# Performance work log

Hardware: AMD Instinct MI355X
Metric: run time of the kernel (lower is better)

The kernel has to match this reference:

```python
import jax, jax.numpy as jnp
import numpy as np

E, K, H, F = 64, 6, 2048, 768        # experts, top_k, hidden, moe_intermediate
G, KG = 8, 4                          # n_group, topk_group
SHARED_F = 768                        # moe_intermediate_size * num_shared_experts
SCALE = 2.5                           # routed_scaling_factor
T = 2 * 1024                          # flattened tokens
CAP = 2 * (T * K // E)


def setup_inputs() -> dict:
    key = jax.random.key(0)
    ks = jax.random.split(key, 9)
    s = 0.02
    return dict(
        hidden_states=jax.random.normal(ks[0], (2, 1024, H), jnp.float32),
        gate_w=jax.random.normal(ks[1], (H, E), jnp.float32) * s,
        bias=jax.random.normal(ks[2], (E,), jnp.float32) * s,          # e_score_correction_bias
        w_gate=jax.random.normal(ks[3], (E, H, F), jnp.float32) * s,
        w_up=jax.random.normal(ks[4], (E, H, F), jnp.float32) * s,
        w_down=jax.random.normal(ks[5], (E, F, H), jnp.float32) * s,
        ws_gate=jax.random.normal(ks[6], (H, SHARED_F), jnp.float32) * s,
        ws_up=jax.random.normal(ks[7], (H, SHARED_F), jnp.float32) * s,
        ws_down=jax.random.normal(ks[8], (SHARED_F, H), jnp.float32) * s,
    )


def _grouped_topk(logits, bias):
    # vLLM grouped_topk with scoring_func='sigmoid' and e_score_correction_bias
    scores = jax.nn.sigmoid(logits.astype(jnp.float32))          # [T, E] original scores
    scores_b = scores + bias[None, :]                            # biased scores for selection
    # group score = sum of top-2 biased scores within each group (bias path)
    gs = scores_b.reshape(-1, G, E // G)
    group_scores = jnp.sum(jax.lax.top_k(gs, 2)[0], axis=-1)     # [T, G]
    gidx = jax.lax.top_k(group_scores, KG)[1]                    # [T, KG]
    rows = jnp.arange(group_scores.shape[0])[:, None]
    group_mask = jnp.zeros_like(group_scores).at[rows, gidx].set(1.0)
    score_mask = jnp.repeat(group_mask, E // G, axis=-1) > 0     # [T, E]
    tmp = jnp.where(score_mask, scores_b, -jnp.inf)
    topk_ids = jax.lax.top_k(tmp, K)[1]                          # [T, K]
    topk_w = jnp.take_along_axis(scores, topk_ids, axis=-1)      # weights from UNBIASED scores
    topk_w = topk_w / jnp.sum(topk_w, axis=-1, keepdims=True)    # renormalize (norm_topk_prob)
    return topk_w * SCALE, topk_ids


def _routed_moe(x, topk_w, topk_ids, w_gate, w_up, w_down):
    Tn = x.shape[0]
    flat_e = topk_ids.reshape(-1)                                # [T*K]
    order = jnp.argsort(flat_e)                                  # stable sort by expert
    se = flat_e[order]                                           # sorted expert ids
    pos = jnp.arange(Tn * K) - jnp.searchsorted(se, se, side='left')  # slot within expert
    tok = order // K                                             # source token per pair
    valid = pos < CAP
    slot = jnp.where(valid, pos, CAP)                            # overflow -> scratch slot
    buf = jnp.zeros((E, CAP + 1, H), x.dtype).at[se, slot].set(x[tok])[:, :CAP]
    h = jax.nn.silu(jnp.einsum('ech,ehf->ecf', buf, w_gate)) * jnp.einsum('ech,ehf->ecf', buf, w_up)
    out = jnp.einsum('ecf,efh->ech', h, w_down)                  # [E, CAP, H]
    gathered = out[se, jnp.minimum(pos, CAP - 1)] * valid.astype(x.dtype)[:, None]
    w = topk_w.reshape(-1)[order].astype(x.dtype)[:, None]
    return jax.ops.segment_sum(gathered * w, tok, num_segments=Tn)


def reference(hidden_states, gate_w, bias, w_gate, w_up, w_down, ws_gate, ws_up, ws_down):
    orig_shape = hidden_states.shape
    x = hidden_states.reshape(-1, H)                             # [T, H]
    router_logits = x @ gate_w                                   # ReplicatedLinear, no bias
    topk_w, topk_ids = _grouped_topk(router_logits, bias)
    y = _routed_moe(x, topk_w, topk_ids, w_gate, w_up, w_down)
    # shared experts: SwiGLU gated MLP
    shared = (jax.nn.silu(x @ ws_gate) * (x @ ws_up)) @ ws_down
    return (y + shared).reshape(orig_shape)
```

## Files before the change

kernel.cpp:

```cpp
#include <hip/hip_runtime.h>
#include <math.h>


#define TOK 2048
#define HD 2048
#define NE 64
#define FD 768
#define TKK 6
#define CAPE 384
#define NG 8
#define KGG 4

typedef float f32x4 __attribute__((ext_vector_type(4)));
typedef short s16x8 __attribute__((ext_vector_type(8)));
typedef short s16x4 __attribute__((ext_vector_type(4)));

__device__ __forceinline__ short f2bf(float f){
  unsigned u = __float_as_uint(f);
  u += 0x7FFFu + ((u >> 16) & 1u);
  return (short)(u >> 16);
}

__global__ void k_convert(const float* __restrict__ x, short* __restrict__ xbf){
  int i = blockIdx.x * 256 + threadIdx.x;
  f32x4 v = ((const f32x4*)x)[i];
  s16x4 o = { f2bf(v[0]), f2bf(v[1]), f2bf(v[2]), f2bf(v[3]) };
  ((s16x4*)xbf)[i] = o;
}

__global__ void k_router(const float* __restrict__ x, const float* __restrict__ gw,
                         float* __restrict__ logits){
  const int t = blockIdx.x * 4 + (threadIdx.x >> 6);
  const int e = threadIdx.x & 63;
  const float* xr = x + (size_t)t * HD;
  float acc = 0.f;
  for (int h = 0; h < HD; h += 4){
    f32x4 xv = *(const f32x4*)(xr + h);
    acc = fmaf(xv[0], gw[(h + 0) * NE + e], acc);
    acc = fmaf(xv[1], gw[(h + 1) * NE + e], acc);
    acc = fmaf(xv[2], gw[(h + 2) * NE + e], acc);
    acc = fmaf(xv[3], gw[(h + 3) * NE + e], acc);
  }
  logits[t * NE + e] = acc;
}

__global__ void k_topk(const float* __restrict__ logits, const float* __restrict__ bias,
                       int* __restrict__ cnt, int* __restrict__ tokl, float* __restrict__ wl){
  const int t = blockIdx.x * 256 + threadIdx.x;
  float sc[NE], sb[NE];
  for (int e = 0; e < NE; ++e){
    float l = logits[t * NE + e];
    float s = 1.f / (1.f + expf(-l));
    sc[e] = s; sb[e] = s + bias[e];
  }
  float gs[NG];
  for (int g = 0; g < NG; ++g){
    float m1 = -1e30f, m2 = -1e30f;
    for (int q = 0; q < 8; ++q){
      float v = sb[g * 8 + q];
      if (v > m1){ m2 = m1; m1 = v; } else if (v > m2){ m2 = v; }
    }
    gs[g] = m1 + m2;
  }
  unsigned gm = 0; unsigned long long allow = 0;
  for (int r = 0; r < KGG; ++r){
    float bb = -1e30f; int bg = 0;
    for (int g = 0; g < NG; ++g)
      if (!((gm >> g) & 1u) && gs[g] > bb){ bb = gs[g]; bg = g; }
    gm |= 1u << bg; allow |= 0xFFull << (bg * 8);
  }
  unsigned long long used = 0; int ids[TKK]; float wv[TKK]; float wsum = 0.f;
  for (int r = 0; r < TKK; ++r){
    float bb = -1e30f; int bi = 0;
    for (int e = 0; e < NE; ++e)
      if (((allow >> e) & 1ull) && !((used >> e) & 1ull) && sb[e] > bb){ bb = sb[e]; bi = e; }
    used |= 1ull << bi; ids[r] = bi;
    float w = sc[bi]; wv[r] = w; wsum += w;
  }
  const float scl = 2.5f / wsum;
  for (int r = 0; r < TKK; ++r){
    int e = ids[r];
    int slot = atomicAdd(cnt + e, 1);
    if (slot < CAPE){ tokl[e * CAPE + slot] = t; wl[e * CAPE + slot] = wv[r] * scl; }
  }
}

template<bool GATHER>
__global__ __launch_bounds__(256, 2) void k_dual(
    const short* __restrict__ xbf,
    const float* __restrict__ Wg, const float* __restrict__ Wu,
    short* __restrict__ hout,
    const int* __restrict__ cnt, const int* __restrict__ tokl)
{
  __shared__ short Asm[256][72];
  __shared__ short Bgs[64][72];
  __shared__ short Bus[64][72];
  const int tid = threadIdx.x;
  const int n0 = blockIdx.x * 64;
  const int m0 = blockIdx.y * 256;
  const int e  = GATHER ? (int)blockIdx.z : 0;
  const int cntc = GATHER ? min(cnt[e], CAPE) : TOK;
  if (m0 >= cntc) return;
  const size_t wb = (size_t)e * HD * FD;
  const float* wg = Wg + wb;
  const float* wu = Wu + wb;

  const int a_r = tid >> 3, a_c = tid & 7;
  const short* arow[8];
#pragma unroll
  for (int p = 0; p < 8; ++p){
    const int gr = m0 + p * 32 + a_r;
    const short* s = nullptr;
    if (gr < cntc){
      const int row = GATHER ? tokl[e * CAPE + gr] : gr;
      s = xbf + (size_t)row * HD;
    }
    arow[p] = s;
  }
  const int b_kg = tid >> 4, b_ng = tid & 15;
  const int lane = tid & 63, wv = tid >> 6;
  const int lm = lane & 15, quad = lane >> 4;

  f32x4 ag[4][4], au[4][4];
#pragma unroll
  for (int i = 0; i < 4; ++i)
#pragma unroll
    for (int j = 0; j < 4; ++j){
      ag[i][j] = {0.f, 0.f, 0.f, 0.f};
      au[i][j] = {0.f, 0.f, 0.f, 0.f};
    }

  for (int k0 = 0; k0 < HD; k0 += 64){
    __syncthreads();
#pragma unroll
    for (int p = 0; p < 8; ++p){
      s16x8 v = {0, 0, 0, 0, 0, 0, 0, 0};
      if (arow[p]) v = *(const s16x8*)(arow[p] + k0 + a_c * 8);
      *(s16x8*)&Asm[p * 32 + a_r][a_c * 8] = v;
    }
    {
      const float* src = wg + (size_t)(k0 + b_kg * 4) * FD + n0 + b_ng * 4;
      f32x4 r0 = *(const f32x4*)(src);
      f32x4 r1 = *(const f32x4*)(src + FD);
      f32x4 r2 = *(const f32x4*)(src + 2 * FD);
      f32x4 r3 = *(const f32x4*)(src + 3 * FD);
#pragma unroll
      for (int c = 0; c < 4; ++c){
        s16x4 v = { f2bf(r0[c]), f2bf(r1[c]), f2bf(r2[c]), f2bf(r3[c]) };
        *(s16x4*)&Bgs[b_ng * 4 + c][b_kg * 4] = v;
      }
      src = wu + (size_t)(k0 + b_kg * 4) * FD + n0 + b_ng * 4;
      r0 = *(const f32x4*)(src);
      r1 = *(const f32x4*)(src + FD);
      r2 = *(const f32x4*)(src + 2 * FD);
      r3 = *(const f32x4*)(src + 3 * FD);
#pragma unroll
      for (int c = 0; c < 4; ++c){
        s16x4 v = { f2bf(r0[c]), f2bf(r1[c]), f2bf(r2[c]), f2bf(r3[c]) };
        *(s16x4*)&Bus[b_ng * 4 + c][b_kg * 4] = v;
      }
    }
    __syncthreads();
#pragma unroll
    for (int s = 0; s < 2; ++s){
      s16x8 af[4], bg[4], bu[4];
#pragma unroll
      for (int i = 0; i < 4; ++i)
        af[i] = *(const s16x8*)&Asm[wv * 64 + i * 16 + lm][s * 32 + quad * 8];
#pragma unroll
      for (int j = 0; j < 4; ++j){
        bg[j] = *(const s16x8*)&Bgs[j * 16 + lm][s * 32 + quad * 8];
        bu[j] = *(const s16x8*)&Bus[j * 16 + lm][s * 32 + quad * 8];
      }
#pragma unroll
      for (int i = 0; i < 4; ++i)
#pragma unroll
        for (int j = 0; j < 4; ++j){
          ag[i][j] = __builtin_amdgcn_mfma_f32_16x16x32_bf16(af[i], bg[j], ag[i][j], 0, 0, 0);
          au[i][j] = __builtin_amdgcn_mfma_f32_16x16x32_bf16(af[i], bu[j], au[i][j], 0, 0, 0);
        }
    }
  }
  const size_t obase = GATHER ? (size_t)e * CAPE : 0;
#pragma unroll
  for (int i = 0; i < 4; ++i){
#pragma unroll
    for (int r = 0; r < 4; ++r){
      const int grow = m0 + wv * 64 + i * 16 + quad * 4 + r;
      if (grow < cntc){
        short* orow = hout + (obase + grow) * FD + n0;
#pragma unroll
        for (int j = 0; j < 4; ++j){
          const float g = ag[i][j][r], u = au[i][j][r];
          const float h = g * u / (1.f + __expf(-g));
          orow[j * 16 + lm] = f2bf(h);
        }
      }
    }
  }
}

template<bool SCATTER>
__global__ __launch_bounds__(256, 2) void k_down(
    const short* __restrict__ hsrc,
    const float* __restrict__ Wd,
    float* __restrict__ out,
    const int* __restrict__ cnt, const int* __restrict__ tokl, const float* __restrict__ wl)
{
  __shared__ short Asm[256][72];
  __shared__ short Bs[64][72];
  const int tid = threadIdx.x;
  const int n0 = blockIdx.x * 64;
  const int m0 = blockIdx.y * 256;
  const int e  = SCATTER ? (int)blockIdx.z : 0;
  const int cntc = SCATTER ? min(cnt[e], CAPE) : TOK;
  if (m0 >= cntc) return;
  const short* abase = hsrc + (size_t)e * CAPE * FD;
  const float* wd = Wd + (size_t)e * FD * HD;

  const int a_r = tid >> 3, a_c = tid & 7;
  const short* arow[8];
#pragma unroll
  for (int p = 0; p < 8; ++p){
    const int gr = m0 + p * 32 + a_r;
    arow[p] = (gr < cntc) ? (abase + (size_t)gr * FD) : nullptr;
  }
  const int b_kg = tid >> 4, b_ng = tid & 15;
  const int lane = tid & 63, wv = tid >> 6;
  const int lm = lane & 15, quad = lane >> 4;

  f32x4 ac[4][4];
#pragma unroll
  for (int i = 0; i < 4; ++i)
#pragma unroll
    for (int j = 0; j < 4; ++j) ac[i][j] = {0.f, 0.f, 0.f, 0.f};

  for (int k0 = 0; k0 < FD; k0 += 64){
    __syncthreads();
#pragma unroll
    for (int p = 0; p < 8; ++p){
      s16x8 v = {0, 0, 0, 0, 0, 0, 0, 0};
      if (arow[p]) v = *(const s16x8*)(arow[p] + k0 + a_c * 8);
      *(s16x8*)&Asm[p * 32 + a_r][a_c * 8] = v;
    }
    {
      const float* src = wd + (size_t)(k0 + b_kg * 4) * HD + n0 + b_ng * 4;
      f32x4 r0 = *(const f32x4*)(src);
      f32x4 r1 = *(const f32x4*)(src + HD);
      f32x4 r2 = *(const f32x4*)(src + 2 * HD);
      f32x4 r3 = *(const f32x4*)(src + 3 * HD);
#pragma unroll
      for (int c = 0; c < 4; ++c){
        s16x4 v = { f2bf(r0[c]), f2bf(r1[c]), f2bf(r2[c]), f2bf(r3[c]) };
        *(s16x4*)&Bs[b_ng * 4 + c][b_kg * 4] = v;
      }
    }
    __syncthreads();
#pragma unroll
    for (int s = 0; s < 2; ++s){
      s16x8 af[4], bf[4];
#pragma unroll
      for (int i = 0; i < 4; ++i)
        af[i] = *(const s16x8*)&Asm[wv * 64 + i * 16 + lm][s * 32 + quad * 8];
#pragma unroll
      for (int j = 0; j < 4; ++j)
        bf[j] = *(const s16x8*)&Bs[j * 16 + lm][s * 32 + quad * 8];
#pragma unroll
      for (int i = 0; i < 4; ++i)
#pragma unroll
        for (int j = 0; j < 4; ++j)
          ac[i][j] = __builtin_amdgcn_mfma_f32_16x16x32_bf16(af[i], bf[j], ac[i][j], 0, 0, 0);
    }
  }
#pragma unroll
  for (int i = 0; i < 4; ++i){
#pragma unroll
    for (int r = 0; r < 4; ++r){
      const int grow = m0 + wv * 64 + i * 16 + quad * 4 + r;
      if (grow < cntc){
        if (SCATTER){
          const int t = tokl[e * CAPE + grow];
          const float w = wl[e * CAPE + grow];
          float* orow = out + (size_t)t * HD + n0;
#pragma unroll
          for (int j = 0; j < 4; ++j)
            atomicAdd(orow + j * 16 + lm, w * ac[i][j][r]);
        } else {
          float* orow = out + (size_t)grow * HD + n0;
#pragma unroll
          for (int j = 0; j < 4; ++j)
            orow[j * 16 + lm] = ac[i][j][r];
        }
      }
    }
  }
}

extern "C" void kernel_launch(void* const* d_in, const int* in_sizes, int n_in,
                              void* d_out, int out_size, void* d_ws, size_t ws_size,
                              hipStream_t stream){
  const float* x    = (const float*)d_in[0];
  const float* gw   = (const float*)d_in[1];
  const float* bias = (const float*)d_in[2];
  const float* wgat = (const float*)d_in[3];
  const float* wup  = (const float*)d_in[4];
  const float* wdn  = (const float*)d_in[5];
  const float* wsg  = (const float*)d_in[6];
  const float* wsu  = (const float*)d_in[7];
  const float* wsd  = (const float*)d_in[8];
  float* out = (float*)d_out;
  char* ws = (char*)d_ws;

  short* xbf    = (short*)(ws);
  short* hbuf   = (short*)(ws + 8388608);
  short* hs     = (short*)(ws + 46137344);
  float* logits = (float*)(ws + 49283072);
  int*   tokl   = (int*)  (ws + 49807360);
  float* wl     = (float*)(ws + 49905664);
  int*   cnt    = (int*)  (ws + 50003968);
  if (ws_size < 50004224) return;

  hipMemsetAsync(cnt, 0, NE * sizeof(int), stream);
  k_convert<<<dim3(TOK * HD / 1024), 256, 0, stream>>>(x, xbf);
  k_router<<<dim3(TOK / 4), 256, 0, stream>>>(x, gw, logits);
  k_topk<<<dim3(TOK / 256), 256, 0, stream>>>(logits, bias, cnt, tokl, wl);
  k_dual<false><<<dim3(FD / 64, TOK / 256, 1), 256, 0, stream>>>(xbf, wsg, wsu, hs, nullptr, nullptr);
  k_down<false><<<dim3(HD / 64, TOK / 256, 1), 256, 0, stream>>>(hs, wsd, out, nullptr, nullptr, nullptr);
  k_dual<true><<<dim3(FD / 64, 2, NE), 256, 0, stream>>>(xbf, wgat, wup, hbuf, cnt, tokl);
  k_down<true><<<dim3(HD / 64, 2, NE), 256, 0, stream>>>(hbuf, wdn, out, cnt, tokl, wl);
}
```

Baseline: 1.680 ms.

## Pipeline global loads, swizzle LDS, shrink M tile, remap blocks across XCDs

Both GEMM kernels now prefetch the next k-slice of activations and weights into registers while MFMAs run on the current slice, and convert the weights to bf16 after the compute step. LDS tiles drop the padded rows and use an XOR swizzle instead to avoid bank conflicts. The M tile shrinks from 256 to 128 rows with a 2x2 wave layout, which roughly doubles the grid and cuts wasted rows for partly filled experts. Block IDs are remapped so that consecutive tiles land on the same XCD. In exchange, the number of fp32 weight reads per output element roughly doubles because each weight tile is reused across fewer rows, and the prefetch registers add register pressure.

Measured after the change: 1.382 ms. -17.7%, faster.

```diff
diff --git a/kernel.cpp b/kernel.cpp
--- a/kernel.cpp
+++ b/kernel.cpp
@@ -19,6 +19,18 @@
   unsigned u = __float_as_uint(f);
   u += 0x7FFFu + ((u >> 16) & 1u);
   return (short)(u >> 16);
+}
+
+__device__ __forceinline__ int lsw(int r, int c){
+  return r * 64 + (((c ^ r ^ (r >> 2)) & 7) << 3);
+}
+
+__device__ __forceinline__ void xcd_decode(int& bx, int& by, int& bz){
+  const int nx = gridDim.x, ny = gridDim.y;
+  const int nwg = nx * ny * gridDim.z;
+  const int lid = blockIdx.x + nx * (blockIdx.y + ny * blockIdx.z);
+  const int wid = (nwg & 7) ? lid : ((lid & 7) * (nwg >> 3) + (lid >> 3));
+  bx = wid % nx; const int r = wid / nx; by = r % ny; bz = r / ny;
 }
 
 __global__ void k_convert(const float* __restrict__ x, short* __restrict__ xbf){
@@ -92,23 +104,24 @@
     short* __restrict__ hout,
     const int* __restrict__ cnt, const int* __restrict__ tokl)
 {
-  __shared__ short Asm[256][72];
-  __shared__ short Bgs[64][72];
-  __shared__ short Bus[64][72];
-  const int tid = threadIdx.x;
-  const int n0 = blockIdx.x * 64;
-  const int m0 = blockIdx.y * 256;
-  const int e  = GATHER ? (int)blockIdx.z : 0;
+  __shared__ __align__(16) short As[128 * 64];
+  __shared__ __align__(16) short Bgs[64 * 64];
+  __shared__ __align__(16) short Bus[64 * 64];
+  int bx, by, bz; xcd_decode(bx, by, bz);
+  const int n0 = bx * 64;
+  const int m0 = by * 128;
+  const int e  = GATHER ? bz : 0;
   const int cntc = GATHER ? min(cnt[e], CAPE) : TOK;
   if (m0 >= cntc) return;
   const size_t wb = (size_t)e * HD * FD;
-  const float* wg = Wg + wb;
-  const float* wu = Wu + wb;
-
+  const float* wg = Wg + wb + n0;
+  const float* wu = Wu + wb + n0;
+
+  const int tid = threadIdx.x;
   const int a_r = tid >> 3, a_c = tid & 7;
-  const short* arow[8];
-#pragma unroll
-  for (int p = 0; p < 8; ++p){
+  const short* arow[4];
+#pragma unroll
+  for (int p = 0; p < 4; ++p){
     const int gr = m0 + p * 32 + a_r;
     const short* s = nullptr;
     if (gr < cntc){
@@ -119,81 +132,98 @@
   }
   const int b_kg = tid >> 4, b_ng = tid & 15;
   const int lane = tid & 63, wv = tid >> 6;
+  const int wm = wv >> 1, wn = wv & 1;
   const int lm = lane & 15, quad = lane >> 4;
 
-  f32x4 ag[4][4], au[4][4];
+  f32x4 ag[4][2], au[4][2];
 #pragma unroll
   for (int i = 0; i < 4; ++i)
 #pragma unroll
-    for (int j = 0; j < 4; ++j){
-      ag[i][j] = {0.f, 0.f, 0.f, 0.f};
-      au[i][j] = {0.f, 0.f, 0.f, 0.f};
-    }
+    for (int j = 0; j < 2; ++j){ ag[i][j] = {0.f,0.f,0.f,0.f}; au[i][j] = {0.f,0.f,0.f,0.f}; }
+
+  s16x8 apf[4];
+  f32x4 gf[4], uf[4];
+  s16x4 gc[4], uc[4];
+  const s16x8 zz = {0,0,0,0,0,0,0,0};
+
+  auto LOADA = [&](int k0){
+#pragma unroll
+    for (int p = 0; p < 4; ++p)
+      apf[p] = arow[p] ? *(const s16x8*)(arow[p] + k0 + a_c * 8) : zz;
+  };
+  auto LOADB = [&](int k0){
+    const float* s1 = wg + (size_t)(k0 + b_kg * 4) * FD + b_ng * 4;
+    gf[0] = *(const f32x4*)(s1);
+    gf[1] = *(const f32x4*)(s1 + FD);
+    gf[2] = *(const f32x4*)(s1 + 2 * FD);
+    gf[3] = *(const f32x4*)(s1 + 3 * FD);
+    const float* s2 = wu + (size_t)(k0 + b_kg * 4) * FD + b_ng * 4;
+    uf[0] = *(const f32x4*)(s2);
+    uf[1] = *(const f32x4*)(s2 + FD);
+    uf[2] = *(const f32x4*)(s2 + 2 * FD);
+    uf[3] = *(const f32x4*)(s2 + 3 * FD);
+  };
+  auto CONVB = [&](){
+#pragma unroll
+    for (int c = 0; c < 4; ++c){
+      s16x4 g4 = { f2bf(gf[0][c]), f2bf(gf[1][c]), f2bf(gf[2][c]), f2bf(gf[3][c]) };
+      s16x4 u4 = { f2bf(uf[0][c]), f2bf(uf[1][c]), f2bf(uf[2][c]), f2bf(uf[3][c]) };
+      gc[c] = g4; uc[c] = u4;
+    }
+  };
+
+  LOADA(0); LOADB(0); CONVB();
 
   for (int k0 = 0; k0 < HD; k0 += 64){
     __syncthreads();
 #pragma unroll
-    for (int p = 0; p < 8; ++p){
-      s16x8 v = {0, 0, 0, 0, 0, 0, 0, 0};
-      if (arow[p]) v = *(const s16x8*)(arow[p] + k0 + a_c * 8);
-      *(s16x8*)&Asm[p * 32 + a_r][a_c * 8] = v;
-    }
-    {
-      const float* src = wg + (size_t)(k0 + b_kg * 4) * FD + n0 + b_ng * 4;
-      f32x4 r0 = *(const f32x4*)(src);
-      f32x4 r1 = *(const f32x4*)(src + FD);
-      f32x4 r2 = *(const f32x4*)(src + 2 * FD);
-      f32x4 r3 = *(const f32x4*)(src + 3 * FD);
-#pragma unroll
-      for (int c = 0; c < 4; ++c){
-        s16x4 v = { f2bf(r0[c]), f2bf(r1[c]), f2bf(r2[c]), f2bf(r3[c]) };
-        *(s16x4*)&Bgs[b_ng * 4 + c][b_kg * 4] = v;
+    for (int p = 0; p < 4; ++p)
+      *(s16x8*)&As[lsw(p * 32 + a_r, a_c)] = apf[p];
+#pragma unroll
+    for (int c = 0; c < 4; ++c){
+      const int n = b_ng * 4 + c;
+      const int off = n * 64 + ((((b_kg >> 1) ^ n ^ (n >> 2)) & 7) << 3) + ((b_kg & 1) << 2);
+      *(s16x4*)&Bgs[off] = gc[c];
+      *(s16x4*)&Bus[off] = uc[c];
+    }
+    __syncthreads();
+    const bool more = (k0 + 64) < HD;
+    if (more){ LOADA(k0 + 64); LOADB(k0 + 64); }
+#pragma unroll
+    for (int s = 0; s < 2; ++s){
+      const int cc = s * 4 + quad;
+      s16x8 af[4], bgr[2], bur[2];
+#pragma unroll
+      for (int i = 0; i < 4; ++i)
+        af[i] = *(const s16x8*)&As[lsw(wm * 64 + i * 16 + lm, cc)];
+#pragma unroll
+      for (int j = 0; j < 2; ++j){
+        bgr[j] = *(const s16x8*)&Bgs[lsw(wn * 32 + j * 16 + lm, cc)];
+        bur[j] = *(const s16x8*)&Bus[lsw(wn * 32 + j * 16 + lm, cc)];
       }
-      src = wu + (size_t)(k0 + b_kg * 4) * FD + n0 + b_ng * 4;
-      r0 = *(const f32x4*)(src);
-      r1 = *(const f32x4*)(src + FD);
-      r2 = *(const f32x4*)(src + 2 * FD);
-      r3 = *(const f32x4*)(src + 3 * FD);
-#pragma unroll
-      for (int c = 0; c < 4; ++c){
-        s16x4 v = { f2bf(r0[c]), f2bf(r1[c]), f2bf(r2[c]), f2bf(r3[c]) };
-        *(s16x4*)&Bus[b_ng * 4 + c][b_kg * 4] = v;
-      }
-    }
-    __syncthreads();
-#pragma unroll
-    for (int s = 0; s < 2; ++s){
-      s16x8 af[4], bg[4], bu[4];
 #pragma unroll
       for (int i = 0; i < 4; ++i)
-        af[i] = *(const s16x8*)&Asm[wv * 64 + i * 16 + lm][s * 32 + quad * 8];
-#pragma unroll
-      for (int j = 0; j < 4; ++j){
-        bg[j] = *(const s16x8*)&Bgs[j * 16 + lm][s * 32 + quad * 8];
-        bu[j] = *(const s16x8*)&Bus[j * 16 + lm][s * 32 + quad * 8];
-      }
-#pragma unroll
-      for (int i = 0; i < 4; ++i)
-#pragma unroll
-        for (int j = 0; j < 4; ++j){
-          ag[i][j] = __builtin_amdgcn_mfma_f32_16x16x32_bf16(af[i], bg[j], ag[i][j], 0, 0, 0);
-          au[i][j] = __builtin_amdgcn_mfma_f32_16x16x32_bf16(af[i], bu[j], au[i][j], 0, 0, 0);
+#pragma unroll
+        for (int j = 0; j < 2; ++j){
+          ag[i][j] = __builtin_amdgcn_mfma_f32_16x16x32_bf16(af[i], bgr[j], ag[i][j], 0, 0, 0);
+          au[i][j] = __builtin_amdgcn_mfma_f32_16x16x32_bf16(af[i], bur[j], au[i][j], 0, 0, 0);
         }
     }
-  }
+    if (more) CONVB();
+  }
+
   const size_t obase = GATHER ? (size_t)e * CAPE : 0;
 #pragma unroll
   for (int i = 0; i < 4; ++i){
 #pragma unroll
     for (int r = 0; r < 4; ++r){
-      const int grow = m0 + wv * 64 + i * 16 + quad * 4 + r;
+      const int grow = m0 + wm * 64 + i * 16 + quad * 4 + r;
       if (grow < cntc){
-        short* orow = hout + (obase + grow) * FD + n0;
-#pragma unroll
-        for (int j = 0; j < 4; ++j){
+        short* orow = hout + (obase + grow) * FD + n0 + wn * 32;
+#pragma unroll
+        for (int j = 0; j < 2; ++j){
           const float g = ag[i][j][r], u = au[i][j][r];
-          const float h = g * u / (1.f + __expf(-g));
-          orow[j * 16 + lm] = f2bf(h);
+          orow[j * 16 + lm] = f2bf(g * u / (1.f + __expf(-g)));
         }
       }
     }
@@ -201,94 +231,119 @@
 }
 
 template<bool SCATTER>
-__global__ __launch_bounds__(256, 2) void k_down(
+__global__ __launch_bounds__(256, 3) void k_down(
     const short* __restrict__ hsrc,
     const float* __restrict__ Wd,
     float* __restrict__ out,
     const int* __restrict__ cnt, const int* __restrict__ tokl, const float* __restrict__ wl)
 {
-  __shared__ short Asm[256][72];
-  __shared__ short Bs[64][72];
-  const int tid = threadIdx.x;
-  const int n0 = blockIdx.x * 64;
-  const int m0 = blockIdx.y * 256;
-  const int e  = SCATTER ? (int)blockIdx.z : 0;
+  __shared__ __align__(16) short As[128 * 64];
+  __shared__ __align__(16) short Bs[64 * 64];
+  int bx, by, bz; xcd_decode(bx, by, bz);
+  const int n0 = bx * 64;
+  const int m0 = by * 128;
+  const int e  = SCATTER ? bz : 0;
   const int cntc = SCATTER ? min(cnt[e], CAPE) : TOK;
   if (m0 >= cntc) return;
   const short* abase = hsrc + (size_t)e * CAPE * FD;
-  const float* wd = Wd + (size_t)e * FD * HD;
-
+  const float* wd = Wd + (size_t)e * FD * HD + n0;
+
+  const int tid = threadIdx.x;
   const int a_r = tid >> 3, a_c = tid & 7;
-  const short* arow[8];
-#pragma unroll
-  for (int p = 0; p < 8; ++p){
+  const short* arow[4];
+#pragma unroll
+  for (int p = 0; p < 4; ++p){
     const int gr = m0 + p * 32 + a_r;
     arow[p] = (gr < cntc) ? (abase + (size_t)gr * FD) : nullptr;
   }
   const int b_kg = tid >> 4, b_ng = tid & 15;
   const int lane = tid & 63, wv = tid >> 6;
+  const int wm = wv >> 1, wn = wv & 1;
   const int lm = lane & 15, quad = lane >> 4;
 
-  f32x4 ac[4][4];
+  f32x4 ac[4][2];
 #pragma unroll
   for (int i = 0; i < 4; ++i)
 #pragma unroll
-    for (int j = 0; j < 4; ++j) ac[i][j] = {0.f, 0.f, 0.f, 0.f};
+    for (int j = 0; j < 2; ++j) ac[i][j] = {0.f,0.f,0.f,0.f};
+
+  s16x8 apf[4];
+  f32x4 df[4];
+  s16x4 dc[4];
+  const s16x8 zz = {0,0,0,0,0,0,0,0};
+
+  auto LOADA = [&](int k0){
+#pragma unroll
+    for (int p = 0; p < 4; ++p)
+      apf[p] = arow[p] ? *(const s16x8*)(arow[p] + k0 + a_c * 8) : zz;
+  };
+  auto LOADB = [&](int k0){
+    const float* s1 = wd + (size_t)(k0 + b_kg * 4) * HD + b_ng * 4;
+    df[0] = *(const f32x4*)(s1);
+    df[1] = *(const f32x4*)(s1 + HD);
+    df[2] = *(const f32x4*)(s1 + 2 * HD);
+    df[3] = *(const f32x4*)(s1 + 3 * HD);
+  };
+  auto CONVB = [&](){
+#pragma unroll
+    for (int c = 0; c < 4; ++c){
+      s16x4 d4 = { f2bf(df[0][c]), f2bf(df[1][c]), f2bf(df[2][c]), f2bf(df[3][c]) };
+      dc[c] = d4;
+    }
+  };
+
+  LOADA(0); LOADB(0); CONVB();
 
   for (int k0 = 0; k0 < FD; k0 += 64){
     __syncthreads();
 #pragma unroll
-    for (int p = 0; p < 8; ++p){
-      s16x8 v = {0, 0, 0, 0, 0, 0, 0, 0};
-      if (arow[p]) v = *(const s16x8*)(arow[p] + k0 + a_c * 8);
-      *(s16x8*)&Asm[p * 32 + a_r][a_c * 8] = v;
-    }
-    {
-      const float* src = wd + (size_t)(k0 + b_kg * 4) * HD + n0 + b_ng * 4;
-      f32x4 r0 = *(const f32x4*)(src);
-      f32x4 r1 = *(const f32x4*)(src + HD);
-      f32x4 r2 = *(const f32x4*)(src + 2 * HD);
-      f32x4 r3 = *(const f32x4*)(src + 3 * HD);
-#pragma unroll
-      for (int c = 0; c < 4; ++c){
-        s16x4 v = { f2bf(r0[c]), f2bf(r1[c]), f2bf(r2[c]), f2bf(r3[c]) };
-        *(s16x4*)&Bs[b_ng * 4 + c][b_kg * 4] = v;
-      }
+    for (int p = 0; p < 4; ++p)
+      *(s16x8*)&As[lsw(p * 32 + a_r, a_c)] = apf[p];
+#pragma unroll
+    for (int c = 0; c < 4; ++c){
+      const int n = b_ng * 4 + c;
+      const int off = n * 64 + ((((b_kg >> 1) ^ n ^ (n >> 2)) & 7) << 3) + ((b_kg & 1) << 2);
+      *(s16x4*)&Bs[off] = dc[c];
     }
     __syncthreads();
+    const bool more = (k0 + 64) < FD;
+    if (more){ LOADA(k0 + 64); LOADB(k0 + 64); }
 #pragma unroll
     for (int s = 0; s < 2; ++s){
-      s16x8 af[4], bf[4];
+      const int cc = s * 4 + quad;
+      s16x8 af[4], bfr[2];
 #pragma unroll
       for (int i = 0; i < 4; ++i)
-        af[i] = *(const s16x8*)&Asm[wv * 64 + i * 16 + lm][s * 32 + quad * 8];
-#pragma unroll
-      for (int j = 0; j < 4; ++j)
-        bf[j] = *(const s16x8*)&Bs[j * 16 + lm][s * 32 + quad * 8];
+        af[i] = *(const s16x8*)&As[lsw(wm * 64 + i * 16 + lm, cc)];
+#pragma unroll
+      for (int j = 0; j < 2; ++j)
+        bfr[j] = *(const s16x8*)&Bs[lsw(wn * 32 + j * 16 + lm, cc)];
 #pragma unroll
       for (int i = 0; i < 4; ++i)
 #pragma unroll
-        for (int j = 0; j < 4; ++j)
-          ac[i][j] = __builtin_amdgcn_mfma_f32_16x16x32_bf16(af[i], bf[j], ac[i][j], 0, 0, 0);
-    }
-  }
+        for (int j = 0; j < 2; ++j)
+          ac[i][j] = __builtin_amdgcn_mfma_f32_16x16x32_bf16(af[i], bfr[j], ac[i][j], 0, 0, 0);
+    }
+    if (more) CONVB();
+  }
+
 #pragma unroll
   for (int i = 0; i < 4; ++i){
 #pragma unroll
     for (int r = 0; r < 4; ++r){
-      const int grow = m0 + wv * 64 + i * 16 + quad * 4 + r;
+      const int grow = m0 + wm * 64 + i * 16 + quad * 4 + r;
       if (grow < cntc){
         if (SCATTER){
           const int t = tokl[e * CAPE + grow];
           const float w = wl[e * CAPE + grow];
-          float* orow = out + (size_t)t * HD + n0;
-#pragma unroll
-          for (int j = 0; j < 4; ++j)
+          float* orow = out + (size_t)t * HD + n0 + wn * 32;
+#pragma unroll
+          for (int j = 0; j < 2; ++j)
             atomicAdd(orow + j * 16 + lm, w * ac[i][j][r]);
         } else {
-          float* orow = out + (size_t)grow * HD + n0;
-#pragma unroll
-          for (int j = 0; j < 4; ++j)
+          float* orow = out + (size_t)grow * HD + n0 + wn * 32;
+#pragma unroll
+          for (int j = 0; j < 2; ++j)
             orow[j * 16 + lm] = ac[i][j][r];
         }
       }
@@ -324,8 +379,8 @@
   k_convert<<<dim3(TOK * HD / 1024), 256, 0, stream>>>(x, xbf);
   k_router<<<dim3(TOK / 4), 256, 0, stream>>>(x, gw, logits);
   k_topk<<<dim3(TOK / 256), 256, 0, stream>>>(logits, bias, cnt, tokl, wl);
-  k_dual<false><<<dim3(FD / 64, TOK / 256, 1), 256, 0, stream>>>(xbf, wsg, wsu, hs, nullptr, nullptr);
-  k_down<false><<<dim3(HD / 64, TOK / 256, 1), 256, 0, stream>>>(hs, wsd, out, nullptr, nullptr, nullptr);
-  k_dual<true><<<dim3(FD / 64, 2, NE), 256, 0, stream>>>(xbf, wgat, wup, hbuf, cnt, tokl);
-  k_down<true><<<dim3(HD / 64, 2, NE), 256, 0, stream>>>(hbuf, wdn, out, cnt, tokl, wl);
-}
+  k_dual<false><<<dim3(FD / 64, TOK / 128, 1), 256, 0, stream>>>(xbf, wsg, wsu, hs, nullptr, nullptr);
+  k_down<false><<<dim3(HD / 64, TOK / 128, 1), 256, 0, stream>>>(hs, wsd, out, nullptr, nullptr, nullptr);
+  k_dual<true><<<dim3(FD / 64, CAPE / 128, NE), 256, 0, stream>>>(xbf, wgat, wup, hbuf, cnt, tokl);
+  k_down<true><<<dim3(HD / 64, CAPE / 128, NE), 256, 0, stream>>>(hbuf, wdn, out, cnt, tokl, wl);
+}
```
